# Kernel optimization log

Measured on AMD Instinct MI355X. Metric: run time of the kernel, lower is better.

## Reference

```python
import jax, jax.numpy as jnp
import numpy as np
from jax import lax


def setup_inputs() -> dict:
    key = jax.random.key(0)
    ks = jax.random.split(key, 10)
    B, T, Din, U = 64, 256, 128, 1024
    def rn(k, shape, sc=0.02):
        return jax.random.normal(k, shape, jnp.float32) * sc
    return {
        "inputs": jax.random.normal(ks[0], (B, T, Din), jnp.float32),
        "We1": rn(ks[1], (Din, U)), "be1": jnp.zeros((U,), jnp.float32),
        "We2": rn(ks[2], (U, U)),   "be2": jnp.zeros((U,), jnp.float32),
        "W1": rn(ks[3], (U, U)),    "b1": jnp.zeros((U,), jnp.float32),
        "W2": rn(ks[4], (U, U)),    "b2": jnp.zeros((U,), jnp.float32),
        "V": rn(ks[5], (U, 1)),     "bV": jnp.zeros((1,), jnp.float32),
        "Wk": rn(ks[6], (U, 4 * U)),
        "Wr": rn(ks[7], (U, 4 * U)),
        "bl": jnp.zeros((4 * U,), jnp.float32),
        "Wo": rn(ks[8], (U, 1)),    "bo": jnp.zeros((1,), jnp.float32),
        "seq_len": 256,
    }


def reference(inputs, We1, be1, We2, be2, W1, b1, W2, b2, V, bV,
              Wk, Wr, bl, Wo, bo, seq_len):
    B = inputs.shape[0]
    U = Wr.shape[0]
    f32 = inputs.dtype
    # Frozen embedding ANN, applied per timestep: [B,T,Din] -> [B,T,U]
    h1 = jax.nn.relu(inputs @ We1 + be1)
    x = jax.nn.relu(h1 @ We2 + be2)            # attention values [B,T,U]
    # W2(values) is constant across decode steps; hoist out of the loop.
    keys = x @ W2 + b2                          # [B,T,U]

    def step(carry, _):
        h, c = carry                            # [B,U] each
        # Bahdanau attention: score = V(tanh(W1(q) + W2(values)))
        q = h @ W1 + b1                         # [B,U]
        score = jnp.tanh(q[:, None, :] + keys) @ V + bV   # [B,T,1]
        attw = jax.nn.softmax(score, axis=1)    # softmax over time axis
        ctx = jnp.sum(attw * x, axis=1)         # context vector [B,U]
        # Keras LSTM cell (gate order i,f,g,o; sigmoid recurrent, tanh act)
        z = ctx @ Wk + h @ Wr + bl              # [B,4U]
        i, f, g, o = jnp.split(z, 4, axis=-1)
        i = jax.nn.sigmoid(i)
        f = jax.nn.sigmoid(f)
        g = jnp.tanh(g)
        o = jax.nn.sigmoid(o)
        c_new = f * c + i * g
        h_new = o * jnp.tanh(c_new)
        out = h_new @ Wo + bo                   # [B,1]
        return (h_new, c_new), out

    init = (jnp.zeros((B, U), f32), jnp.zeros((B, U), f32))
    _, outs = lax.scan(step, init, None, length=seq_len)   # [seq_len,B,1]
    return jnp.squeeze(outs, axis=2)            # [seq_len, B]
```

## Files before the change

### kernel.cpp

```cpp
#include <hip/hip_runtime.h>

#define U_ 1024
#define B_ 64
#define T_ 256
#define DIN_ 128
#define BT_ (B_*T_)
#define G_ 1024
#define NWB 576

#define FA_L   0
#define RELA_L 64
#define CE_L   128
#define CZ_L   192
#define CX_L   208
#define RELX_L 272
#define CC_L   336
#define RELC_L 352
#define SYNC_N (416*16)

typedef __attribute__((ext_vector_type(4))) float f32x4;
typedef __attribute__((ext_vector_type(8))) short s16x8;
typedef __attribute__((ext_vector_type(4))) unsigned short u16x4;
typedef unsigned long long u64;

union U64F2 { u64 q; float f[2]; };
union U64H4 { u64 q; unsigned short h[4]; };

__device__ inline unsigned short f2bf(float x){
  unsigned u = __float_as_uint(x);
  u += 0x7FFFu + ((u >> 16) & 1u);
  return (unsigned short)(u >> 16);
}
__device__ inline float bf2f(unsigned short b){ return __uint_as_float(((unsigned)b) << 16); }
__device__ inline float fast_rcp(float x){ return __builtin_amdgcn_rcpf(x); }
__device__ inline float fast_tanh(float x){
  float e = __expf(2.0f * x);
  return 1.0f - 2.0f * fast_rcp(e + 1.0f);
}
__device__ inline float fast_sig(float x){
  return fast_rcp(1.0f + __expf(-x));
}

__device__ inline u64 ald64(const u64* p){
  return __hip_atomic_load((u64*)p, __ATOMIC_RELAXED, __HIP_MEMORY_SCOPE_AGENT);
}
__device__ inline void ast64(u64* p, u64 v){
  __hip_atomic_store(p, v, __ATOMIC_RELAXED, __HIP_MEMORY_SCOPE_AGENT);
}
__device__ inline float aldf(const float* p){
  return __hip_atomic_load((float*)p, __ATOMIC_RELAXED, __HIP_MEMORY_SCOPE_AGENT);
}
__device__ inline void astf(float* p, float v){
  __hip_atomic_store(p, v, __ATOMIC_RELAXED, __HIP_MEMORY_SCOPE_AGENT);
}
__device__ inline unsigned ald32(const unsigned* p){
  return __hip_atomic_load((unsigned*)p, __ATOMIC_RELAXED, __HIP_MEMORY_SCOPE_AGENT);
}
__device__ inline void ast32(unsigned* p, unsigned v){
  __hip_atomic_store(p, v, __ATOMIC_RELAXED, __HIP_MEMORY_SCOPE_AGENT);
}
__device__ inline void aadd32(unsigned* p, unsigned v){
  __hip_atomic_fetch_add(p, v, __ATOMIC_RELAXED, __HIP_MEMORY_SCOPE_AGENT);
}
__device__ inline s16x8 frag_ald(const u64* p){
  u64 a = ald64(p), b = ald64(p + 1);
  union { u64 q[2]; s16x8 v; } x; x.q[0] = a; x.q[1] = b; return x.v;
}

__device__ inline void wait1(unsigned* line, unsigned tgt){
  if (threadIdx.x == 0){
    while (ald32(line) < tgt) __builtin_amdgcn_s_sleep(2);
  }
  __syncthreads();
}

__device__ inline float score8(s16x8 k0, s16x8 k1, const float* tqv, const float* Vv){
  float s = 0.f;
  #pragma unroll
  for (int e = 0; e < 8; ++e){
    float kf = bf2f((unsigned short)k0[e]);
    float num = tqv[e] + kf;
    float den = fmaf(tqv[e], kf, 1.0f);
    s += Vv[e] * num * fast_rcp(den);
  }
  #pragma unroll
  for (int e = 0; e < 8; ++e){
    float kf = bf2f((unsigned short)k1[e]);
    float num = tqv[8+e] + kf;
    float den = fmaf(tqv[8+e], kf, 1.0f);
    s += Vv[8+e] * num * fast_rcp(den);
  }
  return s;
}

__global__ void init_kernel(float* c, unsigned short* hb0, unsigned short* hb1,
                            unsigned* sync, const float* V, float* vbound){
  int i = blockIdx.x * 256 + threadIdx.x;
  if (i < B_*U_){ c[i] = 0.f; hb0[i] = 0; hb1[i] = 0; }
  if (i < SYNC_N) sync[i] = 0u;
  if (blockIdx.x == 0){
    __shared__ float red[4];
    int t = threadIdx.x, lane = t & 63, w = t >> 6;
    float s = fabsf(V[t]) + fabsf(V[t+256]) + fabsf(V[t+512]) + fabsf(V[t+768]);
    #pragma unroll
    for (int mk = 32; mk >= 1; mk >>= 1) s += __shfl_xor(s, mk, 64);
    if (lane == 0) red[w] = s;
    __syncthreads();
    if (t == 0) vbound[0] = red[0] + red[1] + red[2] + red[3];
  }
}

__global__ void transpose_bf_kernel(const float* W, unsigned short* WT, int K, int N){
  int ktiles = K >> 5;
  int kb = blockIdx.x % ktiles, nb = blockIdx.x / ktiles;
  __shared__ float tile[32][33];
  int x = threadIdx.x & 31, y8 = threadIdx.x >> 5;
  #pragma unroll
  for (int i = 0; i < 4; ++i){
    int y = y8*4 + i;
    tile[y][x] = W[(size_t)(kb*32 + y)*N + nb*32 + x];
  }
  __syncthreads();
  #pragma unroll
  for (int i = 0; i < 4; ++i){
    int y = y8*4 + i;
    WT[(size_t)(nb*32 + y)*K + kb*32 + x] = f2bf(tile[x][y]);
  }
}

template<int AF32>
__global__ __launch_bounds__(256) void gemm_embed(const void* Aptr, const unsigned short* BT,
                                                  const float* bias, unsigned short* Cout,
                                                  int K, int act){
  int nb = blockIdx.x & 15, mb = blockIdx.x >> 4;
  int lane = threadIdx.x & 63, w = threadIdx.x >> 6;
  int l15 = lane & 15, quad = lane >> 4;
  int m0 = mb*64 + w*16;
  int arow = m0 + l15;
  f32x4 acc[4];
  #pragma unroll
  for (int nt = 0; nt < 4; ++nt) acc[nt] = (f32x4){0.f,0.f,0.f,0.f};

  for (int k0 = 0; k0 < K; k0 += 32){
    int koff = k0 + quad*8;
    s16x8 a8;
    if (AF32){
      const float* ap = (const float*)Aptr + (size_t)arow*K + koff;
      f32x4 lo = *(const f32x4*)ap;
      f32x4 hi = *(const f32x4*)(ap + 4);
      a8[0]=(short)f2bf(lo[0]); a8[1]=(short)f2bf(lo[1]); a8[2]=(short)f2bf(lo[2]); a8[3]=(short)f2bf(lo[3]);
      a8[4]=(short)f2bf(hi[0]); a8[5]=(short)f2bf(hi[1]); a8[6]=(short)f2bf(hi[2]); a8[7]=(short)f2bf(hi[3]);
    } else {
      a8 = *(const s16x8*)((const unsigned short*)Aptr + (size_t)arow*K + koff);
    }
    #pragma unroll
    for (int nt = 0; nt < 4; ++nt){
      const unsigned short* bp = BT + (size_t)(nb*64 + nt*16 + l15)*K + koff;
      s16x8 b8 = *(const s16x8*)bp;
      acc[nt] = __builtin_amdgcn_mfma_f32_16x16x32_bf16(a8, b8, acc[nt], 0, 0, 0);
    }
  }
  #pragma unroll
  for (int nt = 0; nt < 4; ++nt){
    int col = nb*64 + nt*16 + l15;
    float bv = bias[col];
    #pragma unroll
    for (int r = 0; r < 4; ++r){
      int row = m0 + quad*4 + r;
      float v = acc[nt][r] + bv;
      v = (act == 0) ? fmaxf(v, 0.f) : fast_tanh(v);
      Cout[(size_t)row*U_ + col] = f2bf(v);
    }
  }
}

struct SeqP {
  const unsigned short *W1Tb, *WkTb, *WrTb, *tk, *xv;
  const float *b1, *bl, *V, *Wo, *bo, *vbound;
  float *tq, *ew, *c, *zh, *out_part, *out;
  unsigned short *ctxb, *hb0, *hb1;
  unsigned *sync;
};

__device__ inline void out_reduce(const SeqP& p, int b, int sidx, float* smem,
                                  int t, int lane, int w){
  float v = aldf(&p.out_part[b*256 + t]);
  #pragma unroll
  for (int mk = 32; mk >= 1; mk >>= 1) v += __shfl_xor(v, mk, 64);
  if (lane == 0) smem[w] = v;
  __syncthreads();
  if (t == 0) p.out[sidx*64 + b] = smem[0] + smem[1] + smem[2] + smem[3] + p.bo[0];
  __syncthreads();
}

__global__ __launch_bounds__(256, 4) void seq_kernel(SeqP p){
  const int bi = blockIdx.x;
  const int t  = threadIdx.x;
  const int lane = t & 63, w = t >> 6;
  const int l15 = lane & 15, quad = lane >> 4;
  __shared__ __align__(16) unsigned short lfrag[16384];
  __shared__ __align__(16) float smem[1664];
  unsigned* sync = p.sync;
  const float Mb = p.vbound[0];

  if (bi < NWB){
    const unsigned short* wsrc;
    if (bi < 64)       wsrc = p.W1Tb + (size_t)(bi*16 + l15)*U_;
    else if (bi < 320) wsrc = p.WrTb + (size_t)((bi - 64)*16 + l15)*U_;
    else               wsrc = p.WkTb + (size_t)((l15 >> 2)*U_ + (bi - 320)*4 + (l15 & 3))*U_;
    for (int it = w; it < 32; it += 4)
      *(s16x8*)&lfrag[it*512 + lane*8] = *(const s16x8*)(wsrc + it*32 + quad*8);
  } else {
    const unsigned short* xsrc = p.xv + (size_t)(bi >> 4)*T_*U_ + (bi & 15)*64;
    #pragma unroll
    for (int it = 0; it < 8; ++it){
      int r = (t >> 3) + 32*it;
      *(s16x8*)&lfrag[r*64 + (t & 7)*8] = *(const s16x8*)(xsrc + (size_t)r*U_ + (t & 7)*8);
    }
  }
  __syncthreads();

  u64* tqu  = (u64*)p.tq;
  u64* ewu  = (u64*)p.ew;
  u64* zhu  = (u64*)p.zh;
  u64* ctxu = (u64*)p.ctxb;

  for (int step = 0; step < T_; ++step){
    const u64* hbRu = (const u64*)((step & 1) ? p.hb1 : p.hb0);
    u64*       hbWu = (u64*)((step & 1) ? p.hb0 : p.hb1);

    if (bi < 64){
      wait1(&sync[(RELC_L + (bi & 63))*16], (unsigned)step);
      int jcol = bi*16 + l15;
      int rbase = (w*16 + l15) << 8;
      f32x4 acc = (f32x4){0.f,0.f,0.f,0.f};
      #pragma unroll 8
      for (int k = 0; k < U_; k += 32){
        s16x8 a8 = frag_ald(hbRu + rbase + ((k + quad*8) >> 2));
        s16x8 b8 = *(const s16x8*)&lfrag[(k >> 5)*512 + lane*8];
        acc = __builtin_amdgcn_mfma_f32_16x16x32_bf16(a8, b8, acc, 0, 0, 0);
      }
      float bj = p.b1[jcol];
      float* tqs = smem;
      #pragma unroll
      for (int r = 0; r < 4; ++r)
        tqs[l15*68 + w*16 + quad*4 + r] = fast_tanh(acc[r] + bj);
      __syncthreads();
      if (t < 64){
        int ub64 = (t*U_ + bi*16) >> 1;
        #pragma unroll
        for (int cc = 0; cc < 16; cc += 2){
          U64F2 x;
          x.f[0] = tqs[(cc+0)*68 + t];
          x.f[1] = tqs[(cc+1)*68 + t];
          ast64(tqu + ub64 + (cc >> 1), x.q);
        }
      }
      __syncthreads();
      if (t == 0) ast32(&sync[(FA_L + bi)*16], (unsigned)(step + 1));
      if (bi == 0){
        if (t < 64){
          unsigned tgt = (unsigned)(step + 1);
          for (;;){
            bool ok = ald32(&sync[(FA_L + t)*16]) >= tgt;
            if (__ballot(ok) == ~0ull) break;
            __builtin_amdgcn_s_sleep(1);
          }
          ast32(&sync[(RELA_L + t)*16], tgt);
        }
      }
    } else if (bi < 320){
      wait1(&sync[(RELC_L + (bi & 63))*16], (unsigned)step);
      int bz = bi - 64;
      int rbase = (w*16 + l15) << 8;
      int jc0 = bz*16 + l15;
      f32x4 acc0 = (f32x4){0.f,0.f,0.f,0.f};
      #pragma unroll 8
      for (int k = 0; k < U_; k += 32){
        s16x8 a8 = frag_ald(hbRu + rbase + ((k + quad*8) >> 2));
        s16x8 b8 = *(const s16x8*)&lfrag[(k >> 5)*512 + lane*8];
        acc0 = __builtin_amdgcn_mfma_f32_16x16x32_bf16(a8, b8, acc0, 0, 0, 0);
      }
      float bl0 = p.bl[jc0];
      int brow = w*16 + quad*4;
      U64F2 x;
      int i0 = (jc0*64 + brow) >> 1;
      x.f[0] = acc0[0] + bl0; x.f[1] = acc0[1] + bl0; ast64(zhu + i0, x.q);
      x.f[0] = acc0[2] + bl0; x.f[1] = acc0[3] + bl0; ast64(zhu + i0 + 1, x.q);
      __syncthreads();
      if (t == 0) aadd32(&sync[(CZ_L + ((bi - 64) & 15))*16], 1u);
    } else if (bi >= 960){
      if (bi == 960){
        if (step > 0){
          if (t < 64){
            unsigned tgt = 16u * (unsigned)step;
            for (;;){
              bool ok = (t < 16) ? (ald32(&sync[(CC_L + t)*16]) >= tgt) : true;
              if (__ballot(ok) == ~0ull) break;
              __builtin_amdgcn_s_sleep(1);
            }
            ast32(&sync[(RELC_L + t)*16], (unsigned)step);
          }
          __syncthreads();
          out_reduce(p, 0, step - 1, smem, t, lane, w);
        }
      } else {
        wait1(&sync[(RELC_L + (bi & 63))*16], (unsigned)step);
        if (step > 0) out_reduce(p, bi - 960, step - 1, smem, t, lane, w);
      }
    }

    wait1(&sync[(RELA_L + (bi & 63))*16], (unsigned)(step + 1));
    {
      int b = bi >> 4, tg = bi & 15;
      float tqv[16], Vv[16];
      int tqb = (b*U_ + lane*16) >> 1;
      #pragma unroll
      for (int i = 0; i < 8; ++i){
        U64F2 x; x.q = ald64(tqu + tqb + i);
        tqv[2*i] = x.f[0]; tqv[2*i+1] = x.f[1];
      }
      const float* Vp = p.V + lane*16;
      #pragma unroll
      for (int i = 0; i < 16; i += 4) *(f32x4*)&Vv[i] = *(const f32x4*)(Vp + i);
      int trow = tg*16 + w*4;
      float sr[4];
      const unsigned short* kp = p.tk + (size_t)(b*T_ + trow)*U_ + lane*16;
      #pragma unroll
      for (int rr = 0; rr < 4; ++rr){
        s16x8 k0 = *(const s16x8*)(kp + (size_t)rr*U_);
        s16x8 k1 = *(const s16x8*)(kp + (size_t)rr*U_ + 8);
        sr[rr] = score8(k0, k1, tqv, Vv);
      }
      #pragma unroll
      for (int mk = 32; mk >= 1; mk >>= 1){
        #pragma unroll
        for (int rr = 0; rr < 4; ++rr) sr[rr] += __shfl_xor(sr[rr], mk, 64);
      }
      if (lane == 0){
        int eb = (b*T_ + trow) >> 1;
        #pragma unroll
        for (int j = 0; j < 2; ++j){
          U64F2 x;
          x.f[0] = __expf(sr[2*j]   - Mb);
          x.f[1] = __expf(sr[2*j+1] - Mb);
          ast64(ewu + eb + j, x.q);
        }
      }
    }
    __syncthreads();
    if (t == 0) aadd32(&sync[(CE_L + (bi >> 4))*16], 1u);

    wait1(&sync[(CE_L + (bi >> 4))*16], 16u * (unsigned)(step + 1));
    {
      int b = bi >> 4, ug = bi & 15;
      float* ewL = smem;
      float* tmp = smem + 256;
      float* red = smem + 272;
      if (t < 128){
        U64F2 x; x.q = ald64(ewu + b*128 + t);
        ewL[2*t] = x.f[0]; ewL[2*t+1] = x.f[1];
      }
      __syncthreads();
      float e = ewL[t];
      float sum = e;
      #pragma unroll
      for (int mk = 32; mk >= 1; mk >>= 1) sum += __shfl_xor(sum, mk, 64);
      if (lane == 0) tmp[w] = sum;
      __syncthreads();
      float rd = fast_rcp(tmp[0] + tmp[1] + tmp[2] + tmp[3]);

      int ui = t & 15, tgp = t >> 4;
      f32x4 a = (f32x4){0.f,0.f,0.f,0.f};
      if (bi >= NWB){
        #pragma unroll 4
        for (int t8 = tgp; t8 < T_; t8 += 16){
          float wg = ewL[t8];
          u16x4 x4 = *(const u16x4*)&lfrag[t8*64 + ui*4];
          a[0] = fmaf(wg, bf2f(x4[0]), a[0]);
          a[1] = fmaf(wg, bf2f(x4[1]), a[1]);
          a[2] = fmaf(wg, bf2f(x4[2]), a[2]);
          a[3] = fmaf(wg, bf2f(x4[3]), a[3]);
        }
      } else {
        int u = ug*64 + ui*4;
        const unsigned short* xp = p.xv + (size_t)b*T_*U_ + u;
        #pragma unroll 4
        for (int t8 = tgp; t8 < T_; t8 += 16){
          float wg = ewL[t8];
          u16x4 x4 = *(const u16x4*)(xp + (size_t)t8*U_);
          a[0] = fmaf(wg, bf2f(x4[0]), a[0]);
          a[1] = fmaf(wg, bf2f(x4[1]), a[1]);
          a[2] = fmaf(wg, bf2f(x4[2]), a[2]);
          a[3] = fmaf(wg, bf2f(x4[3]), a[3]);
        }
      }
      *(f32x4*)&red[(tgp*16 + ui)*4] = a;
      __syncthreads();
      if (t < 16){
        f32x4 r = (f32x4){0.f,0.f,0.f,0.f};
        #pragma unroll
        for (int g = 0; g < 16; ++g){
          f32x4 rr = *(f32x4*)&red[(g*16 + t)*4];
          r[0]+=rr[0]; r[1]+=rr[1]; r[2]+=rr[2]; r[3]+=rr[3];
        }
        U64H4 cv;
        cv.h[0]=f2bf(r[0]*rd); cv.h[1]=f2bf(r[1]*rd); cv.h[2]=f2bf(r[2]*rd); cv.h[3]=f2bf(r[3]*rd);
        ast64(ctxu + b*256 + ug*16 + t, cv.q);
      }
    }
    __syncthreads();
    if (t == 0) aadd32(&sync[(CX_L + (bi & 63))*16], 1u);

    if (bi == 576){
      unsigned tgt = 16u * (unsigned)(step + 1);
      if (w == 0){
        for (;;){
          bool ok = ald32(&sync[(CX_L + lane)*16]) >= tgt;
          if (__ballot(ok) == ~0ull) break;
          __builtin_amdgcn_s_sleep(1);
        }
      } else if (w == 1){
        for (;;){
          bool ok = (lane < 16) ? (ald32(&sync[(CZ_L + lane)*16]) >= tgt) : true;
          if (__ballot(ok) == ~0ull) break;
          __builtin_amdgcn_s_sleep(1);
        }
      }
      __syncthreads();
      if (t < 64) ast32(&sync[(RELX_L + t)*16], (unsigned)(step + 1));
    }

    if (bi >= 320 && bi < NWB){
      wait1(&sync[(RELX_L + (bi & 63))*16], (unsigned)(step + 1));
      int cb = bi - 320;
      int ub = cb*4;
      int gate = l15 >> 2, uo = l15 & 3;
      int jcol = gate*U_ + ub + uo;
      int rbase = (w*16 + l15) << 8;
      f32x4 acc = (f32x4){0.f,0.f,0.f,0.f};
      #pragma unroll 8
      for (int k = 0; k < U_; k += 32){
        s16x8 a8 = frag_ald(ctxu + rbase + ((k + quad*8) >> 2));
        acc = __builtin_amdgcn_mfma_f32_16x16x32_bf16(a8, *(const s16x8*)&lfrag[(k >> 5)*512 + lane*8], acc, 0, 0, 0);
      }
      int brow = w*16 + quad*4;
      int zi0 = (jcol*64 + brow) >> 1;
      U64F2 z0, z1;
      z0.q = ald64(zhu + zi0); z1.q = ald64(zhu + zi0 + 1);
      acc[0] += z0.f[0]; acc[1] += z0.f[1]; acc[2] += z1.f[0]; acc[3] += z1.f[1];
      float* zs = smem;
      float* hs = smem + 1088;
      float* op = smem + 1344;
      *(f32x4*)&zs[l15*68 + brow] = acc;
      __syncthreads();
      {
        int b = t & 63, ui = t >> 6;
        int u = ub + ui;
        float zi = zs[(0*4 + ui)*68 + b];
        float zf = zs[(1*4 + ui)*68 + b];
        float zg = zs[(2*4 + ui)*68 + b];
        float zo = zs[(3*4 + ui)*68 + b];
        float ig = fast_sig(zi), fg = fast_sig(zf);
        float gg = fast_tanh(zg), og = fast_sig(zo);
        float cold = p.c[u*64 + b];
        float cn = fg*cold + ig*gg;
        float hn = og * fast_tanh(cn);
        p.c[u*64 + b] = cn;
        hs[ui*64 + b] = hn;
        op[ui*64 + b] = hn * p.Wo[u];
      }
      __syncthreads();
      if (t < 64){
        U64H4 h0;
        #pragma unroll
        for (int k = 0; k < 4; ++k) h0.h[k] = f2bf(hs[k*64 + t]);
        ast64(hbWu + t*256 + cb, h0.q);
        float po = op[t] + op[64 + t] + op[128 + t] + op[192 + t];
        astf(&p.out_part[t*256 + cb], po);
      }
      __syncthreads();
      if (t == 0) aadd32(&sync[(CC_L + ((bi - 320) & 15))*16], 1u);
    }
  }

  if (bi == 960){
    if (t < 64){
      unsigned tgt = 16u * (unsigned)T_;
      for (;;){
        bool ok = (t < 16) ? (ald32(&sync[(CC_L + t)*16]) >= tgt) : true;
        if (__ballot(ok) == ~0ull) break;
        __builtin_amdgcn_s_sleep(1);
      }
      ast32(&sync[(RELC_L + t)*16], (unsigned)T_);
    }
    __syncthreads();
    out_reduce(p, 0, T_ - 1, smem, t, lane, w);
  } else if (bi > 960){
    wait1(&sync[(RELC_L + (bi & 63))*16], (unsigned)T_);
    out_reduce(p, bi - 960, T_ - 1, smem, t, lane, w);
  }
}

extern "C" void kernel_launch(void* const* d_in, const int* in_sizes, int n_in,
                              void* d_out, int out_size, void* d_ws, size_t ws_size,
                              hipStream_t stream){
  const float* inputs = (const float*)d_in[0];
  const float* We1 = (const float*)d_in[1];
  const float* be1 = (const float*)d_in[2];
  const float* We2 = (const float*)d_in[3];
  const float* be2 = (const float*)d_in[4];
  const float* W1  = (const float*)d_in[5];
  const float* b1  = (const float*)d_in[6];
  const float* W2  = (const float*)d_in[7];
  const float* b2  = (const float*)d_in[8];
  const float* V   = (const float*)d_in[9];
  const float* Wk  = (const float*)d_in[11];
  const float* Wr  = (const float*)d_in[12];
  const float* bl  = (const float*)d_in[13];
  const float* Wo  = (const float*)d_in[14];
  const float* bo  = (const float*)d_in[15];
  float* out = (float*)d_out;

  char* ws = (char*)d_ws;
  size_t off = 0;
  auto alloc = [&](size_t bytes) -> void* {
    void* pp = ws + off;
    off = (off + bytes + 255) & ~(size_t)255;
    return pp;
  };
  unsigned short* We1Tb = (unsigned short*)alloc((size_t)1024*128*2);
  unsigned short* We2Tb = (unsigned short*)alloc((size_t)1024*1024*2);
  unsigned short* W2Tb  = (unsigned short*)alloc((size_t)1024*1024*2);
  unsigned short* W1Tb  = (unsigned short*)alloc((size_t)1024*1024*2);
  unsigned short* WkTb  = (unsigned short*)alloc((size_t)4096*1024*2);
  unsigned short* WrTb  = (unsigned short*)alloc((size_t)4096*1024*2);
  unsigned short* h1tk  = (unsigned short*)alloc((size_t)BT_*U_*2);
  unsigned short* xv    = (unsigned short*)alloc((size_t)BT_*U_*2);
  float*          c     = (float*)alloc((size_t)B_*U_*4);
  unsigned short* hb0   = (unsigned short*)alloc((size_t)B_*U_*2);
  unsigned short* hb1   = (unsigned short*)alloc((size_t)B_*U_*2);
  unsigned short* ctxb  = (unsigned short*)alloc((size_t)B_*U_*2);
  float*          tq    = (float*)alloc((size_t)B_*U_*4);
  float*          ew    = (float*)alloc((size_t)B_*T_*4);
  float*          zh    = (float*)alloc((size_t)4*U_*64*4);
  float*          out_part = (float*)alloc((size_t)64*256*4);
  unsigned*       sync  = (unsigned*)alloc((size_t)SYNC_N*4);
  float*          vbound= (float*)alloc(256);
  if (ws_size < off) return;

  init_kernel<<<256, 256, 0, stream>>>(c, hb0, hb1, sync, V, vbound);
  transpose_bf_kernel<<<(128/32)*(1024/32),  256, 0, stream>>>(We1, We1Tb, 128, 1024);
  transpose_bf_kernel<<<(1024/32)*(1024/32), 256, 0, stream>>>(We2, We2Tb, 1024, 1024);
  transpose_bf_kernel<<<(1024/32)*(1024/32), 256, 0, stream>>>(W2,  W2Tb,  1024, 1024);
  transpose_bf_kernel<<<(1024/32)*(1024/32), 256, 0, stream>>>(W1,  W1Tb,  1024, 1024);
  transpose_bf_kernel<<<(1024/32)*(4096/32), 256, 0, stream>>>(Wk,  WkTb,  1024, 4096);
  transpose_bf_kernel<<<(1024/32)*(4096/32), 256, 0, stream>>>(Wr,  WrTb,  1024, 4096);

  gemm_embed<1><<<4096, 256, 0, stream>>>((const void*)inputs, We1Tb, be1, h1tk, DIN_, 0);
  gemm_embed<0><<<4096, 256, 0, stream>>>((const void*)h1tk,   We2Tb, be2, xv,   U_,   0);
  gemm_embed<0><<<4096, 256, 0, stream>>>((const void*)xv,     W2Tb,  b2,  h1tk, U_,   1);

  SeqP sp;
  sp.W1Tb = W1Tb; sp.WkTb = WkTb; sp.WrTb = WrTb; sp.tk = h1tk; sp.xv = xv;
  sp.b1 = b1; sp.bl = bl; sp.V = V; sp.Wo = Wo; sp.bo = bo; sp.vbound = vbound;
  sp.tq = tq; sp.ew = ew; sp.c = c; sp.zh = zh;
  sp.out_part = out_part; sp.out = out;
  sp.ctxb = ctxb; sp.hb0 = hb0; sp.hb1 = hb1; sp.sync = sync;
  seq_kernel<<<dim3(G_), dim3(256), 0, stream>>>(sp);
}
```

Before: 12.17 ms.

## Pipeline persistent LSTM-attention decode across four batch groups with per-group sync

Splits the 64-row batch into four groups of 16. Each phase (query projection, recurrent gate GEMM, attention, context gate GEMM) now runs per group with its own sync counters, so different groups can sit in different phases at once. Each block is assigned a fixed interleaved schedule of phases across groups. The per-block GEMMs become split-K across waves with a shared-memory reduction, output partials are double-buffered, and the dedicated output blocks are removed. The aim is to overlap the serial phase chain and shorten idle time between grid barriers, at the cost of more sync traffic and a more fragile ordering that could deadlock or reduce per-phase efficiency.

Result: slower. 15.70 ms (+29.0%).

```diff
diff --git a/kernel.cpp b/kernel.cpp
--- a/kernel.cpp
+++ b/kernel.cpp
@@ -6,17 +6,18 @@
 #define DIN_ 128
 #define BT_ (B_*T_)
 #define G_ 1024
-#define NWB 576
-
-#define FA_L   0
-#define RELA_L 64
-#define CE_L   128
-#define CZ_L   192
-#define CX_L   208
-#define RELX_L 272
-#define CC_L   336
-#define RELC_L 352
-#define SYNC_N (416*16)
+#define NG 4
+#define XVB 576
+
+#define FA_L    0
+#define RELA_L  256
+#define CE_L    512
+#define CZ_L    576
+#define CX_L    640
+#define RELX_L  704
+#define CC_L    960
+#define RELC_L  1024
+#define SYNC_N  (1280*16)
 
 typedef __attribute__((ext_vector_type(4))) float f32x4;
 typedef __attribute__((ext_vector_type(8))) short s16x8;
@@ -182,28 +183,18 @@
   unsigned *sync;
 };
 
-__device__ inline void out_reduce(const SeqP& p, int b, int sidx, float* smem,
-                                  int t, int lane, int w){
-  float v = aldf(&p.out_part[b*256 + t]);
-  #pragma unroll
-  for (int mk = 32; mk >= 1; mk >>= 1) v += __shfl_xor(v, mk, 64);
-  if (lane == 0) smem[w] = v;
-  __syncthreads();
-  if (t == 0) p.out[sidx*64 + b] = smem[0] + smem[1] + smem[2] + smem[3] + p.bo[0];
-  __syncthreads();
-}
-
 __global__ __launch_bounds__(256, 4) void seq_kernel(SeqP p){
   const int bi = blockIdx.x;
   const int t  = threadIdx.x;
   const int lane = t & 63, w = t >> 6;
   const int l15 = lane & 15, quad = lane >> 4;
+  const int b_own = bi >> 4, tg_own = bi & 15, g_own = bi >> 8;
   __shared__ __align__(16) unsigned short lfrag[16384];
   __shared__ __align__(16) float smem[1664];
   unsigned* sync = p.sync;
   const float Mb = p.vbound[0];
 
-  if (bi < NWB){
+  if (bi < XVB){
     const unsigned short* wsrc;
     if (bi < 64)       wsrc = p.W1Tb + (size_t)(bi*16 + l15)*U_;
     else if (bi < 320) wsrc = p.WrTb + (size_t)((bi - 64)*16 + l15)*U_;
@@ -211,7 +202,7 @@
     for (int it = w; it < 32; it += 4)
       *(s16x8*)&lfrag[it*512 + lane*8] = *(const s16x8*)(wsrc + it*32 + quad*8);
   } else {
-    const unsigned short* xsrc = p.xv + (size_t)(bi >> 4)*T_*U_ + (bi & 15)*64;
+    const unsigned short* xsrc = p.xv + (size_t)b_own*T_*U_ + tg_own*64;
     #pragma unroll
     for (int it = 0; it < 8; ++it){
       int r = (t >> 3) + 32*it;
@@ -222,99 +213,83 @@
 
   u64* tqu  = (u64*)p.tq;
   u64* ewu  = (u64*)p.ew;
-  u64* zhu  = (u64*)p.zh;
   u64* ctxu = (u64*)p.ctxb;
 
   for (int step = 0; step < T_; ++step){
     const u64* hbRu = (const u64*)((step & 1) ? p.hb1 : p.hb0);
     u64*       hbWu = (u64*)((step & 1) ? p.hb0 : p.hb1);
 
-    if (bi < 64){
-      wait1(&sync[(RELC_L + (bi & 63))*16], (unsigned)step);
-      int jcol = bi*16 + l15;
-      int rbase = (w*16 + l15) << 8;
+    auto OUTD = [&](int sidx){
+      float v = aldf(&p.out_part[(sidx & 1)*16384 + b_own*256 + t]);
+      #pragma unroll
+      for (int mk = 32; mk >= 1; mk >>= 1) v += __shfl_xor(v, mk, 64);
+      if (lane == 0) smem[w] = v;
+      __syncthreads();
+      if (t == 0) p.out[sidx*64 + b_own] = smem[0] + smem[1] + smem[2] + smem[3] + p.bo[0];
+      __syncthreads();
+    };
+
+    auto PH_A = [&](int g){
+      wait1(&sync[(RELC_L + g*64 + (bi & 63))*16], (unsigned)step);
       f32x4 acc = (f32x4){0.f,0.f,0.f,0.f};
-      #pragma unroll 8
-      for (int k = 0; k < U_; k += 32){
-        s16x8 a8 = frag_ald(hbRu + rbase + ((k + quad*8) >> 2));
-        s16x8 b8 = *(const s16x8*)&lfrag[(k >> 5)*512 + lane*8];
-        acc = __builtin_amdgcn_mfma_f32_16x16x32_bf16(a8, b8, acc, 0, 0, 0);
-      }
-      float bj = p.b1[jcol];
-      float* tqs = smem;
-      #pragma unroll
-      for (int r = 0; r < 4; ++r)
-        tqs[l15*68 + w*16 + quad*4 + r] = fast_tanh(acc[r] + bj);
-      __syncthreads();
+      #pragma unroll
+      for (int i = 0; i < 8; ++i){
+        int k = w*256 + i*32;
+        s16x8 a8 = frag_ald(hbRu + (g*16 + l15)*256 + ((k + quad*8) >> 2));
+        acc = __builtin_amdgcn_mfma_f32_16x16x32_bf16(a8, *(const s16x8*)&lfrag[(k >> 5)*512 + lane*8], acc, 0, 0, 0);
+      }
+      #pragma unroll
+      for (int r = 0; r < 4; ++r) smem[w*256 + (quad*4 + r)*16 + l15] = acc[r];
+      __syncthreads();
+      {
+        int m = t >> 4, col = t & 15;
+        int jcol = bi*16 + col;
+        float v = smem[t] + smem[256+t] + smem[512+t] + smem[768+t] + p.b1[jcol];
+        astf(&p.tq[(size_t)(g*16 + m)*U_ + jcol], fast_tanh(v));
+      }
+      __syncthreads();
+      if (t == 0) ast32(&sync[(FA_L + g*64 + bi)*16], (unsigned)(step + 1));
+    };
+
+    auto AGGA = [&](int g){
       if (t < 64){
-        int ub64 = (t*U_ + bi*16) >> 1;
-        #pragma unroll
-        for (int cc = 0; cc < 16; cc += 2){
-          U64F2 x;
-          x.f[0] = tqs[(cc+0)*68 + t];
-          x.f[1] = tqs[(cc+1)*68 + t];
-          ast64(tqu + ub64 + (cc >> 1), x.q);
-        }
-      }
-      __syncthreads();
-      if (t == 0) ast32(&sync[(FA_L + bi)*16], (unsigned)(step + 1));
-      if (bi == 0){
-        if (t < 64){
-          unsigned tgt = (unsigned)(step + 1);
-          for (;;){
-            bool ok = ald32(&sync[(FA_L + t)*16]) >= tgt;
-            if (__ballot(ok) == ~0ull) break;
-            __builtin_amdgcn_s_sleep(1);
-          }
-          ast32(&sync[(RELA_L + t)*16], tgt);
-        }
-      }
-    } else if (bi < 320){
-      wait1(&sync[(RELC_L + (bi & 63))*16], (unsigned)step);
-      int bz = bi - 64;
-      int rbase = (w*16 + l15) << 8;
-      int jc0 = bz*16 + l15;
-      f32x4 acc0 = (f32x4){0.f,0.f,0.f,0.f};
-      #pragma unroll 8
-      for (int k = 0; k < U_; k += 32){
-        s16x8 a8 = frag_ald(hbRu + rbase + ((k + quad*8) >> 2));
-        s16x8 b8 = *(const s16x8*)&lfrag[(k >> 5)*512 + lane*8];
-        acc0 = __builtin_amdgcn_mfma_f32_16x16x32_bf16(a8, b8, acc0, 0, 0, 0);
-      }
-      float bl0 = p.bl[jc0];
-      int brow = w*16 + quad*4;
-      U64F2 x;
-      int i0 = (jc0*64 + brow) >> 1;
-      x.f[0] = acc0[0] + bl0; x.f[1] = acc0[1] + bl0; ast64(zhu + i0, x.q);
-      x.f[0] = acc0[2] + bl0; x.f[1] = acc0[3] + bl0; ast64(zhu + i0 + 1, x.q);
-      __syncthreads();
-      if (t == 0) aadd32(&sync[(CZ_L + ((bi - 64) & 15))*16], 1u);
-    } else if (bi >= 960){
-      if (bi == 960){
-        if (step > 0){
-          if (t < 64){
-            unsigned tgt = 16u * (unsigned)step;
-            for (;;){
-              bool ok = (t < 16) ? (ald32(&sync[(CC_L + t)*16]) >= tgt) : true;
-              if (__ballot(ok) == ~0ull) break;
-              __builtin_amdgcn_s_sleep(1);
-            }
-            ast32(&sync[(RELC_L + t)*16], (unsigned)step);
-          }
-          __syncthreads();
-          out_reduce(p, 0, step - 1, smem, t, lane, w);
-        }
-      } else {
-        wait1(&sync[(RELC_L + (bi & 63))*16], (unsigned)step);
-        if (step > 0) out_reduce(p, bi - 960, step - 1, smem, t, lane, w);
-      }
-    }
-
-    wait1(&sync[(RELA_L + (bi & 63))*16], (unsigned)(step + 1));
-    {
-      int b = bi >> 4, tg = bi & 15;
+        unsigned tgt = (unsigned)(step + 1);
+        for (;;){
+          bool ok = ald32(&sync[(FA_L + g*64 + t)*16]) >= tgt;
+          if (__ballot(ok) == ~0ull) break;
+          __builtin_amdgcn_s_sleep(1);
+        }
+        ast32(&sync[(RELA_L + g*64 + t)*16], tgt);
+      }
+    };
+
+    auto PH_Z = [&](int g){
+      wait1(&sync[(RELC_L + g*64 + (bi & 63))*16], (unsigned)step);
+      f32x4 acc = (f32x4){0.f,0.f,0.f,0.f};
+      #pragma unroll
+      for (int i = 0; i < 8; ++i){
+        int k = w*256 + i*32;
+        s16x8 a8 = frag_ald(hbRu + (g*16 + l15)*256 + ((k + quad*8) >> 2));
+        acc = __builtin_amdgcn_mfma_f32_16x16x32_bf16(a8, *(const s16x8*)&lfrag[(k >> 5)*512 + lane*8], acc, 0, 0, 0);
+      }
+      #pragma unroll
+      for (int r = 0; r < 4; ++r) smem[w*256 + (quad*4 + r)*16 + l15] = acc[r];
+      __syncthreads();
+      {
+        int m = t >> 4, col = t & 15;
+        int jcol = (bi - 64)*16 + col;
+        float v = smem[t] + smem[256+t] + smem[512+t] + smem[768+t] + p.bl[jcol];
+        astf(&p.zh[jcol*64 + g*16 + m], v);
+      }
+      __syncthreads();
+      if (t == 0) aadd32(&sync[(CZ_L + g*16 + ((bi - 64) & 15))*16], 1u);
+    };
+
+    auto B1 = [&](){
+      int g = g_own;
+      wait1(&sync[(RELA_L + g*64 + (bi & 63))*16], (unsigned)(step + 1));
       float tqv[16], Vv[16];
-      int tqb = (b*U_ + lane*16) >> 1;
+      int tqb = (b_own*U_ + lane*16) >> 1;
       #pragma unroll
       for (int i = 0; i < 8; ++i){
         U64F2 x; x.q = ald64(tqu + tqb + i);
@@ -323,9 +298,9 @@
       const float* Vp = p.V + lane*16;
       #pragma unroll
       for (int i = 0; i < 16; i += 4) *(f32x4*)&Vv[i] = *(const f32x4*)(Vp + i);
-      int trow = tg*16 + w*4;
+      int trow = tg_own*16 + w*4;
       float sr[4];
-      const unsigned short* kp = p.tk + (size_t)(b*T_ + trow)*U_ + lane*16;
+      const unsigned short* kp = p.tk + (size_t)(b_own*T_ + trow)*U_ + lane*16;
       #pragma unroll
       for (int rr = 0; rr < 4; ++rr){
         s16x8 k0 = *(const s16x8*)(kp + (size_t)rr*U_);
@@ -338,7 +313,7 @@
         for (int rr = 0; rr < 4; ++rr) sr[rr] += __shfl_xor(sr[rr], mk, 64);
       }
       if (lane == 0){
-        int eb = (b*T_ + trow) >> 1;
+        int eb = (b_own*T_ + trow) >> 1;
         #pragma unroll
         for (int j = 0; j < 2; ++j){
           U64F2 x;
@@ -347,18 +322,17 @@
           ast64(ewu + eb + j, x.q);
         }
       }
-    }
-    __syncthreads();
-    if (t == 0) aadd32(&sync[(CE_L + (bi >> 4))*16], 1u);
-
-    wait1(&sync[(CE_L + (bi >> 4))*16], 16u * (unsigned)(step + 1));
-    {
-      int b = bi >> 4, ug = bi & 15;
+      __syncthreads();
+      if (t == 0) aadd32(&sync[(CE_L + b_own)*16], 1u);
+    };
+
+    auto B2 = [&](){
+      wait1(&sync[(CE_L + b_own)*16], 16u * (unsigned)(step + 1));
       float* ewL = smem;
       float* tmp = smem + 256;
       float* red = smem + 272;
       if (t < 128){
-        U64F2 x; x.q = ald64(ewu + b*128 + t);
+        U64F2 x; x.q = ald64(ewu + b_own*128 + t);
         ewL[2*t] = x.f[0]; ewL[2*t+1] = x.f[1];
       }
       __syncthreads();
@@ -372,7 +346,7 @@
 
       int ui = t & 15, tgp = t >> 4;
       f32x4 a = (f32x4){0.f,0.f,0.f,0.f};
-      if (bi >= NWB){
+      if (bi >= XVB){
         #pragma unroll 4
         for (int t8 = tgp; t8 < T_; t8 += 16){
           float wg = ewL[t8];
@@ -383,8 +357,8 @@
           a[3] = fmaf(wg, bf2f(x4[3]), a[3]);
         }
       } else {
-        int u = ug*64 + ui*4;
-        const unsigned short* xp = p.xv + (size_t)b*T_*U_ + u;
+        int u = tg_own*64 + ui*4;
+        const unsigned short* xp = p.xv + (size_t)b_own*T_*U_ + u;
         #pragma unroll 4
         for (int t8 = tgp; t8 < T_; t8 += 16){
           float wg = ewL[t8];
@@ -400,105 +374,145 @@
       if (t < 16){
         f32x4 r = (f32x4){0.f,0.f,0.f,0.f};
         #pragma unroll
-        for (int g = 0; g < 16; ++g){
-          f32x4 rr = *(f32x4*)&red[(g*16 + t)*4];
+        for (int g2 = 0; g2 < 16; ++g2){
+          f32x4 rr = *(f32x4*)&red[(g2*16 + t)*4];
           r[0]+=rr[0]; r[1]+=rr[1]; r[2]+=rr[2]; r[3]+=rr[3];
         }
         U64H4 cv;
         cv.h[0]=f2bf(r[0]*rd); cv.h[1]=f2bf(r[1]*rd); cv.h[2]=f2bf(r[2]*rd); cv.h[3]=f2bf(r[3]*rd);
-        ast64(ctxu + b*256 + ug*16 + t, cv.q);
-      }
-    }
-    __syncthreads();
-    if (t == 0) aadd32(&sync[(CX_L + (bi & 63))*16], 1u);
-
-    if (bi == 576){
-      unsigned tgt = 16u * (unsigned)(step + 1);
-      if (w == 0){
+        ast64(ctxu + b_own*256 + tg_own*16 + t, cv.q);
+      }
+      __syncthreads();
+      if (t == 0) aadd32(&sync[(CX_L + g_own*16 + tg_own)*16], 1u);
+    };
+
+    auto AGGX = [&](int g){
+      if (t < 64){
+        unsigned tgt = 16u * (unsigned)(step + 1);
         for (;;){
-          bool ok = ald32(&sync[(CX_L + lane)*16]) >= tgt;
+          bool ok = (lane < 16) ? (ald32(&sync[(CX_L + g*16 + lane)*16]) >= tgt)
+                  : (lane < 32) ? (ald32(&sync[(CZ_L + g*16 + (lane-16))*16]) >= tgt)
+                  : true;
           if (__ballot(ok) == ~0ull) break;
           __builtin_amdgcn_s_sleep(1);
         }
-      } else if (w == 1){
+        ast32(&sync[(RELX_L + g*64 + t)*16], (unsigned)(step + 1));
+      }
+    };
+
+    auto PH_C = [&](int g){
+      wait1(&sync[(RELX_L + g*64 + (bi & 63))*16], (unsigned)(step + 1));
+      int cb = bi - 320, ub = cb*4;
+      f32x4 acc = (f32x4){0.f,0.f,0.f,0.f};
+      #pragma unroll
+      for (int i = 0; i < 8; ++i){
+        int k = w*256 + i*32;
+        s16x8 a8 = frag_ald(ctxu + (g*16 + l15)*256 + ((k + quad*8) >> 2));
+        acc = __builtin_amdgcn_mfma_f32_16x16x32_bf16(a8, *(const s16x8*)&lfrag[(k >> 5)*512 + lane*8], acc, 0, 0, 0);
+      }
+      #pragma unroll
+      for (int r = 0; r < 4; ++r) smem[w*256 + (quad*4 + r)*16 + l15] = acc[r];
+      __syncthreads();
+      float* zs2 = smem + 1024;
+      float* hs  = smem + 1280;
+      float* op  = smem + 1344;
+      {
+        int m = t >> 4, col = t & 15;
+        int jcol = (col >> 2)*U_ + ub + (col & 3);
+        float z = smem[t] + smem[256+t] + smem[512+t] + smem[768+t]
+                + aldf(&p.zh[jcol*64 + g*16 + m]);
+        zs2[col*16 + m] = z;
+      }
+      __syncthreads();
+      if (t < 64){
+        int boff = t & 15, ui = t >> 4;
+        float zi = zs2[(0*4 + ui)*16 + boff];
+        float zf = zs2[(1*4 + ui)*16 + boff];
+        float zg = zs2[(2*4 + ui)*16 + boff];
+        float zo = zs2[(3*4 + ui)*16 + boff];
+        float ig = fast_sig(zi), fg = fast_sig(zf);
+        float gg = fast_tanh(zg), og = fast_sig(zo);
+        int u = ub + ui, bg = g*16 + boff;
+        float cold = p.c[u*64 + bg];
+        float cn = fg*cold + ig*gg;
+        float hn = og * fast_tanh(cn);
+        p.c[u*64 + bg] = cn;
+        hs[ui*16 + boff] = hn;
+        op[ui*16 + boff] = hn * p.Wo[u];
+      }
+      __syncthreads();
+      if (t < 16){
+        int bg = g*16 + t;
+        U64H4 h0;
+        #pragma unroll
+        for (int k = 0; k < 4; ++k) h0.h[k] = f2bf(hs[k*16 + t]);
+        ast64(hbWu + bg*256 + cb, h0.q);
+        float po = op[t] + op[16 + t] + op[32 + t] + op[48 + t];
+        astf(&p.out_part[(step & 1)*16384 + bg*256 + cb], po);
+      }
+      __syncthreads();
+      if (t == 0) aadd32(&sync[(CC_L + g*16 + (cb & 15))*16], 1u);
+    };
+
+    auto AGGC = [&](int g){
+      if (t < 64){
+        unsigned tgt = 16u * (unsigned)(step + 1);
         for (;;){
-          bool ok = (lane < 16) ? (ald32(&sync[(CZ_L + lane)*16]) >= tgt) : true;
+          bool ok = (lane < 16) ? (ald32(&sync[(CC_L + g*16 + lane)*16]) >= tgt) : true;
           if (__ballot(ok) == ~0ull) break;
           __builtin_amdgcn_s_sleep(1);
         }
-      }
-      __syncthreads();
-      if (t < 64) ast32(&sync[(RELX_L + t)*16], (unsigned)(step + 1));
+        ast32(&sync[(RELC_L + g*64 + t)*16], (unsigned)(step + 1));
+      }
+    };
+
+    if (tg_own == 15 && step > 0){
+      wait1(&sync[(RELC_L + g_own*64 + (bi & 63))*16], (unsigned)step);
+      OUTD(step - 1);
     }
 
-    if (bi >= 320 && bi < NWB){
-      wait1(&sync[(RELX_L + (bi & 63))*16], (unsigned)(step + 1));
-      int cb = bi - 320;
-      int ub = cb*4;
-      int gate = l15 >> 2, uo = l15 & 3;
-      int jcol = gate*U_ + ub + uo;
-      int rbase = (w*16 + l15) << 8;
-      f32x4 acc = (f32x4){0.f,0.f,0.f,0.f};
-      #pragma unroll 8
-      for (int k = 0; k < U_; k += 32){
-        s16x8 a8 = frag_ald(ctxu + rbase + ((k + quad*8) >> 2));
-        acc = __builtin_amdgcn_mfma_f32_16x16x32_bf16(a8, *(const s16x8*)&lfrag[(k >> 5)*512 + lane*8], acc, 0, 0, 0);
-      }
-      int brow = w*16 + quad*4;
-      int zi0 = (jcol*64 + brow) >> 1;
-      U64F2 z0, z1;
-      z0.q = ald64(zhu + zi0); z1.q = ald64(zhu + zi0 + 1);
-      acc[0] += z0.f[0]; acc[1] += z0.f[1]; acc[2] += z1.f[0]; acc[3] += z1.f[1];
-      float* zs = smem;
-      float* hs = smem + 1088;
-      float* op = smem + 1344;
-      *(f32x4*)&zs[l15*68 + brow] = acc;
-      __syncthreads();
-      {
-        int b = t & 63, ui = t >> 6;
-        int u = ub + ui;
-        float zi = zs[(0*4 + ui)*68 + b];
-        float zf = zs[(1*4 + ui)*68 + b];
-        float zg = zs[(2*4 + ui)*68 + b];
-        float zo = zs[(3*4 + ui)*68 + b];
-        float ig = fast_sig(zi), fg = fast_sig(zf);
-        float gg = fast_tanh(zg), og = fast_sig(zo);
-        float cold = p.c[u*64 + b];
-        float cn = fg*cold + ig*gg;
-        float hn = og * fast_tanh(cn);
-        p.c[u*64 + b] = cn;
-        hs[ui*64 + b] = hn;
-        op[ui*64 + b] = hn * p.Wo[u];
-      }
-      __syncthreads();
-      if (t < 64){
-        U64H4 h0;
-        #pragma unroll
-        for (int k = 0; k < 4; ++k) h0.h[k] = f2bf(hs[k*64 + t]);
-        ast64(hbWu + t*256 + cb, h0.q);
-        float po = op[t] + op[64 + t] + op[128 + t] + op[192 + t];
-        astf(&p.out_part[t*256 + cb], po);
-      }
-      __syncthreads();
-      if (t == 0) aadd32(&sync[(CC_L + ((bi - 320) & 15))*16], 1u);
+    if (bi < 64){
+      PH_A(0); if (bi == 0) AGGA(0);
+      B1(); B2(); if (bi == 0) AGGX(0);
+      PH_A(1); if (bi == 1) AGGA(1);
+      PH_A(2); if (bi == 2) AGGA(2);
+      PH_A(3); if (bi == 3) AGGA(3);
+    } else if (bi < 256){
+      PH_Z(0);
+      B1(); B2();
+      PH_Z(1); PH_Z(2); PH_Z(3);
+      if (bi == 65) AGGC(0);
+    } else if (bi < 320){
+      PH_Z(0); PH_Z(1);
+      B1(); B2(); if (bi == 256) AGGX(1);
+      PH_Z(2); PH_Z(3);
+      if (bi == 257) AGGC(1);
+    } else if (bi < 512){
+      B1(); B2();
+      PH_C(0); PH_C(1); PH_C(2); PH_C(3);
+    } else if (bi < 576){
+      PH_C(0);
+      B1(); B2();
+      PH_C(1); PH_C(2); PH_C(3);
+    } else if (bi < 768){
+      B1(); B2();
+      if (bi == 576) AGGX(2);
+      if (bi == 577) AGGC(2);
+    } else {
+      B1(); B2();
+      if (bi == 768) AGGX(3);
+      if (bi == 769) AGGC(3);
     }
   }
 
-  if (bi == 960){
-    if (t < 64){
-      unsigned tgt = 16u * (unsigned)T_;
-      for (;;){
-        bool ok = (t < 16) ? (ald32(&sync[(CC_L + t)*16]) >= tgt) : true;
-        if (__ballot(ok) == ~0ull) break;
-        __builtin_amdgcn_s_sleep(1);
-      }
-      ast32(&sync[(RELC_L + t)*16], (unsigned)T_);
-    }
+  if (tg_own == 15){
+    wait1(&sync[(RELC_L + g_own*64 + (bi & 63))*16], (unsigned)T_);
+    float v = aldf(&p.out_part[((T_-1) & 1)*16384 + b_own*256 + t]);
+    #pragma unroll
+    for (int mk = 32; mk >= 1; mk >>= 1) v += __shfl_xor(v, mk, 64);
+    if (lane == 0) smem[w] = v;
     __syncthreads();
-    out_reduce(p, 0, T_ - 1, smem, t, lane, w);
-  } else if (bi > 960){
-    wait1(&sync[(RELC_L + (bi & 63))*16], (unsigned)T_);
-    out_reduce(p, bi - 960, T_ - 1, smem, t, lane, w);
+    if (t == 0) p.out[(T_-1)*64 + b_own] = smem[0] + smem[1] + smem[2] + smem[3] + p.bo[0];
   }
 }
 
@@ -544,7 +558,7 @@
   float*          tq    = (float*)alloc((size_t)B_*U_*4);
   float*          ew    = (float*)alloc((size_t)B_*T_*4);
   float*          zh    = (float*)alloc((size_t)4*U_*64*4);
-  float*          out_part = (float*)alloc((size_t)64*256*4);
+  float*          out_part = (float*)alloc((size_t)2*64*256*4);
   unsigned*       sync  = (unsigned*)alloc((size_t)SYNC_N*4);
   float*          vbound= (float*)alloc(256);
   if (ws_size < off) return;
```

## Replace two-hop relay barriers with direct counter polling by all consumer blocks

Applied to the files above, without the earlier changes.

Removes the relay blocks (bi==960 for CC and bi==576 for CX/CZ) that aggregated completion counters and then republished release flags. Every consumer block now polls the 16 or 64 counter lines directly with a wave-wide ballot. This removes one cross-block hop of latency from each per-step barrier in the 256-step recurrence. In exchange, hundreds of blocks poll the same cache lines, which adds contention on those lines.

New measurement: 13.27 ms. 9.0% more time.

```diff
diff --git a/kernel.cpp b/kernel.cpp
--- a/kernel.cpp
+++ b/kernel.cpp
@@ -13,9 +13,7 @@
 #define CE_L   128
 #define CZ_L   192
 #define CX_L   208
-#define RELX_L 272
 #define CC_L   336
-#define RELC_L 352
 #define SYNC_N (416*16)
 
 typedef __attribute__((ext_vector_type(4))) float f32x4;
@@ -70,6 +68,34 @@
 __device__ inline void wait1(unsigned* line, unsigned tgt){
   if (threadIdx.x == 0){
     while (ald32(line) < tgt) __builtin_amdgcn_s_sleep(2);
+  }
+  __syncthreads();
+}
+
+__device__ inline void waitCC(unsigned* sync, unsigned tgt, int lane, int w){
+  if (w == 0){
+    for (;;){
+      bool ok = (lane < 16) ? (ald32(&sync[(CC_L + lane)*16]) >= tgt) : true;
+      if (__ballot(ok) == ~0ull) break;
+      __builtin_amdgcn_s_sleep(1);
+    }
+  }
+  __syncthreads();
+}
+
+__device__ inline void waitXZ(unsigned* sync, unsigned tgt, int lane, int w){
+  if (w == 0){
+    for (;;){
+      bool ok = ald32(&sync[(CX_L + lane)*16]) >= tgt;
+      if (__ballot(ok) == ~0ull) break;
+      __builtin_amdgcn_s_sleep(1);
+    }
+  } else if (w == 1){
+    for (;;){
+      bool ok = (lane < 16) ? (ald32(&sync[(CZ_L + lane)*16]) >= tgt) : true;
+      if (__ballot(ok) == ~0ull) break;
+      __builtin_amdgcn_s_sleep(1);
+    }
   }
   __syncthreads();
 }
@@ -230,7 +256,7 @@
     u64*       hbWu = (u64*)((step & 1) ? p.hb0 : p.hb1);
 
     if (bi < 64){
-      wait1(&sync[(RELC_L + (bi & 63))*16], (unsigned)step);
+      waitCC(sync, 16u * (unsigned)step, lane, w);
       int jcol = bi*16 + l15;
       int rbase = (w*16 + l15) << 8;
       f32x4 acc = (f32x4){0.f,0.f,0.f,0.f};
@@ -270,7 +296,7 @@
         }
       }
     } else if (bi < 320){
-      wait1(&sync[(RELC_L + (bi & 63))*16], (unsigned)step);
+      waitCC(sync, 16u * (unsigned)step, lane, w);
       int bz = bi - 64;
       int rbase = (w*16 + l15) << 8;
       int jc0 = bz*16 + l15;
@@ -290,24 +316,8 @@
       __syncthreads();
       if (t == 0) aadd32(&sync[(CZ_L + ((bi - 64) & 15))*16], 1u);
     } else if (bi >= 960){
-      if (bi == 960){
-        if (step > 0){
-          if (t < 64){
-            unsigned tgt = 16u * (unsigned)step;
-            for (;;){
-              bool ok = (t < 16) ? (ald32(&sync[(CC_L + t)*16]) >= tgt) : true;
-              if (__ballot(ok) == ~0ull) break;
-              __builtin_amdgcn_s_sleep(1);
-            }
-            ast32(&sync[(RELC_L + t)*16], (unsigned)step);
-          }
-          __syncthreads();
-          out_reduce(p, 0, step - 1, smem, t, lane, w);
-        }
-      } else {
-        wait1(&sync[(RELC_L + (bi & 63))*16], (unsigned)step);
-        if (step > 0) out_reduce(p, bi - 960, step - 1, smem, t, lane, w);
-      }
+      waitCC(sync, 16u * (unsigned)step, lane, w);
+      if (step > 0) out_reduce(p, bi - 960, step - 1, smem, t, lane, w);
     }
 
     wait1(&sync[(RELA_L + (bi & 63))*16], (unsigned)(step + 1));
@@ -412,27 +422,8 @@
     __syncthreads();
     if (t == 0) aadd32(&sync[(CX_L + (bi & 63))*16], 1u);
 
-    if (bi == 576){
-      unsigned tgt = 16u * (unsigned)(step + 1);
-      if (w == 0){
-        for (;;){
-          bool ok = ald32(&sync[(CX_L + lane)*16]) >= tgt;
-          if (__ballot(ok) == ~0ull) break;
-          __builtin_amdgcn_s_sleep(1);
-        }
-      } else if (w == 1){
-        for (;;){
-          bool ok = (lane < 16) ? (ald32(&sync[(CZ_L + lane)*16]) >= tgt) : true;
-          if (__ballot(ok) == ~0ull) break;
-          __builtin_amdgcn_s_sleep(1);
-        }
-      }
-      __syncthreads();
-      if (t < 64) ast32(&sync[(RELX_L + t)*16], (unsigned)(step + 1));
-    }
-
     if (bi >= 320 && bi < NWB){
-      wait1(&sync[(RELX_L + (bi & 63))*16], (unsigned)(step + 1));
+      waitXZ(sync, 16u * (unsigned)(step + 1), lane, w);
       int cb = bi - 320;
       int ub = cb*4;
       int gate = l15 >> 2, uo = l15 & 3;
@@ -484,20 +475,8 @@
     }
   }
 
-  if (bi == 960){
-    if (t < 64){
-      unsigned tgt = 16u * (unsigned)T_;
-      for (;;){
-        bool ok = (t < 16) ? (ald32(&sync[(CC_L + t)*16]) >= tgt) : true;
-        if (__ballot(ok) == ~0ull) break;
-        __builtin_amdgcn_s_sleep(1);
-      }
-      ast32(&sync[(RELC_L + t)*16], (unsigned)T_);
-    }
-    __syncthreads();
-    out_reduce(p, 0, T_ - 1, smem, t, lane, w);
-  } else if (bi > 960){
-    wait1(&sync[(RELC_L + (bi & 63))*16], (unsigned)T_);
+  if (bi >= 960){
+    waitCC(sync, 16u * (unsigned)T_, lane, w);
     out_reduce(p, bi - 960, T_ - 1, smem, t, lane, w);
   }
 }
```
